# Optimization experiments

Measured on AMD Instinct MI355X. Metric: run time of the kernel, lower is better.

## Reference

```python
import jax, jax.numpy as jnp
import numpy as np

HW = 24       # image_size // patch_size
HEAD = 16     # vision num_attention_heads
B, T, C, H = 8, 8, 1024, 4096


def _sincos_1d(d, pos):
    omega = np.arange(d // 2, dtype=np.float32) / (d / 2.0)
    omega = 1.0 / 10000 ** omega
    out = np.einsum('m,d->md', pos.reshape(-1).astype(np.float32), omega)
    return np.concatenate([np.sin(out), np.cos(out)], axis=1)


def _pos_embed_3d(embed_dim, grid_size, t_size):
    ds = embed_dim // 4 * 3
    dt = embed_dim // 4
    gh = np.arange(grid_size, dtype=np.float32)
    grid = np.stack(np.meshgrid(gh, gh), axis=0).reshape(2, -1)  # (w, h) order as in source
    spatial = np.concatenate([_sincos_1d(ds // 2, grid[0]), _sincos_1d(ds // 2, grid[1])], axis=1)  # [g*g, ds]
    temporal = _sincos_1d(dt, np.arange(t_size, dtype=np.float32))  # [t, dt]
    spatial = np.repeat(spatial[np.newaxis], t_size, axis=0)                 # [t, g*g, ds]
    temporal = np.repeat(temporal[:, np.newaxis], grid_size ** 2, axis=1)    # [t, g*g, dt]
    emb = np.concatenate([temporal, spatial], axis=-1)
    return emb.reshape(1, t_size * grid_size ** 2, embed_dim).astype(np.float32)


def setup_inputs() -> dict:
    key = jax.random.key(0)
    k1, k2, k3 = jax.random.split(key, 3)
    x = jax.random.normal(k1, (B, T * HW * HW, C), dtype=jnp.float32)
    W1 = jax.random.normal(k2, (C, H), dtype=jnp.float32) * 0.02
    b1 = jnp.zeros((H,), jnp.float32)
    W2 = jax.random.normal(k3, (H, H), dtype=jnp.float32) * 0.02
    b2 = jnp.zeros((H,), jnp.float32)
    pos_embed = jnp.asarray(_pos_embed_3d(C, HW, T))
    return {"x": x, "pos_embed": pos_embed, "W1": W1, "b1": b1, "W2": W2, "b2": b2,
            "local_num_frames": T}


def _merge(x, unm_idx, src_idx, dst_idx):
    # ToMe merge: gather unmatched src tokens, scatter-add matched src into dst.
    src, dst = x[:, ::2], x[:, 1::2]
    unm = jnp.take_along_axis(src, unm_idx[:, :, None], axis=1)   # [b, t1-r, c]
    sel = jnp.take_along_axis(src, src_idx[:, :, None], axis=1)   # [b, r, c]
    dst = jax.vmap(lambda d, i, s: d.at[i].add(s))(dst, dst_idx, sel)
    return jnp.concatenate([unm, dst], axis=1)


def _merge_tokens(x, target, head):
    b, p, c = x.shape
    # static merge schedule (same logic as torch merge_tokens)
    rs, tmp = [], p
    while tmp != target:
        if tmp - target <= tmp // 2:
            rs.append(tmp - target)
            break
        rs.append(tmp // 2)
        tmp -= tmp // 2
    dim = c // head
    size = jnp.ones((b, p, 1), x.dtype)
    for r in rs:
        bb, pp, _ = x.shape
        # metric/index computation is under no_grad in the original
        metric = jax.lax.stop_gradient(x).reshape(bb, pp, head, dim).mean(2)
        metric = metric / jnp.linalg.norm(metric, axis=-1, keepdims=True)
        a_m, b_m = metric[:, ::2], metric[:, 1::2]
        scores = jnp.einsum('bic,bjc->bij', a_m, b_m)  # [b, ta, tb]
        node_max = scores.max(-1)
        node_idx = scores.argmax(-1)
        edge_idx = jnp.argsort(-node_max, axis=-1)      # descending
        unm_idx, src_idx = edge_idx[:, r:], edge_idx[:, :r]
        dst_idx = jnp.take_along_axis(node_idx, src_idx, axis=1)
        # weighted-average merge (merge_wavg)
        x = _merge(x * size, unm_idx, src_idx, dst_idx)
        size = _merge(size, unm_idx, src_idx, dst_idx)
        x = x / size
    return x


def reference(x, pos_embed, W1, b1, W2, b2, local_num_frames):
    x = x + pos_embed.astype(x.dtype)
    x = _merge_tokens(x, local_num_frames * 16, HEAD)
    h = jax.nn.gelu(x @ W1 + b1, approximate=False)  # nn.GELU() is exact erf gelu
    return h @ W2 + b2
```

## Files before the change

### kernel.cpp

```cpp
#include <hip/hip_runtime.h>
#include <hip/hip_bf16.h>
#include <math.h>
#include <stdint.h>

typedef unsigned short u16;
typedef __attribute__((ext_vector_type(8))) short short8;
typedef __attribute__((ext_vector_type(4))) float floatx4;

#define NB 8
#define P0 4608
#define C0 1024
#define H0 4096

__global__ void detect_mode_kernel(const uint32_t* __restrict__ pe_words, int* __restrict__ mode) {
  *mode = (pe_words[64] != 0u) ? 1 : 0;
}

__device__ __forceinline__ float load_in(const void* p, size_t idx, int mode) {
  if (mode) return __bfloat162float(((const __hip_bfloat16*)p)[idx]);
  return ((const float*)p)[idx];
}

__device__ __forceinline__ float4 load4(const void* p, size_t idx, int mode) {
  float4 r;
  if (mode) {
    ushort4 u = *(const ushort4*)((const u16*)p + idx);
    r.x = __bfloat162float(*(__hip_bfloat16*)&u.x);
    r.y = __bfloat162float(*(__hip_bfloat16*)&u.y);
    r.z = __bfloat162float(*(__hip_bfloat16*)&u.z);
    r.w = __bfloat162float(*(__hip_bfloat16*)&u.w);
  } else {
    r = *(const float4*)((const float*)p + idx);
  }
  return r;
}

__device__ __forceinline__ void write_hilo(u16* __restrict__ m2, size_t tok, int lane, float v) {
  __hip_bfloat16 hi = __float2bfloat16(v);
  float hif = __bfloat162float(hi);
  __hip_bfloat16 lo = __float2bfloat16(v - hif);
  m2[tok * 128 + lane] = *(u16*)&hi;
  m2[tok * 128 + 64 + lane] = *(u16*)&lo;
}

__global__ void metric_in_kernel(const void* __restrict__ x, const void* __restrict__ pos,
                                 const int* __restrict__ mode, u16* __restrict__ m2) {
  int tok = blockIdx.x * 4 + (threadIdx.x >> 6);
  int lane = threadIdx.x & 63;
  if (tok >= NB * P0) return;
  int b = tok / P0, t = tok - b * P0;
  int md = *mode;
  size_t xbase = ((size_t)b * P0 + t) * C0 + lane;
  size_t pbase = (size_t)t * C0 + lane;
  float s = 0.f;
#pragma unroll
  for (int h = 0; h < 16; ++h)
    s += load_in(x, xbase + h * 64, md) + load_in(pos, pbase + h * 64, md);
  s *= (1.f / 16.f);
  float sq = s * s;
#pragma unroll
  for (int off = 1; off < 64; off <<= 1) sq += __shfl_xor(sq, off, 64);
  write_hilo(m2, (size_t)tok, lane, s / sqrtf(sq));
}

__global__ void metric_f32_kernel(const float* __restrict__ x, u16* __restrict__ m2, int p) {
  int tok = blockIdx.x * 4 + (threadIdx.x >> 6);
  int lane = threadIdx.x & 63;
  if (tok >= NB * p) return;
  const float* xr = x + (size_t)tok * C0 + lane;
  float s = 0.f;
#pragma unroll
  for (int h = 0; h < 16; ++h) s += xr[h * 64];
  s *= (1.f / 16.f);
  float sq = s * s;
#pragma unroll
  for (int off = 1; off < 64; off <<= 1) sq += __shfl_xor(sq, off, 64);
  write_hilo(m2, (size_t)tok, lane, s / sqrtf(sq));
}

__global__ __launch_bounds__(256) void score_mfma_kernel(const u16* __restrict__ M2,
                                                         int p, int p2, int jT2,
                                                         float* __restrict__ pm,
                                                         int* __restrict__ pi) {
  const int bi = blockIdx.x, ii = blockIdx.y, b = blockIdx.z;
  const int t = threadIdx.x, w = t >> 6, L = t & 63;
  const int wr = w >> 1, wc = w & 1;
  const int fr = L & 15, fo = (L >> 4) * 8;
  const u16* Mb = M2 + (size_t)b * p * 128;

  floatx4 acc[4][4];
#pragma unroll
  for (int mt = 0; mt < 4; ++mt)
#pragma unroll
    for (int nt = 0; nt < 4; ++nt) acc[mt][nt] = (floatx4){0.f, 0.f, 0.f, 0.f};

  const u16* arp[4];
  const u16* brp[4];
#pragma unroll
  for (int mt = 0; mt < 4; ++mt) {
    int i = ii * 128 + wr * 64 + mt * 16 + fr;
    int ta = 2 * i;
    if (ta > p - 2) ta = p - 2;
    arp[mt] = Mb + (size_t)ta * 128 + fo;
    int j = bi * 128 + wc * 64 + mt * 16 + fr;
    int tb = 2 * j + 1;
    if (tb > p - 1) tb = p - 1;
    brp[mt] = Mb + (size_t)tb * 128 + fo;
  }

#pragma unroll
  for (int ks = 0; ks < 2; ++ks) {
    short8 ah[4], al[4], bh[4], bl[4];
#pragma unroll
    for (int mt = 0; mt < 4; ++mt) {
      ah[mt] = *(const short8*)(arp[mt] + ks * 32);
      al[mt] = *(const short8*)(arp[mt] + ks * 32 + 64);
      bh[mt] = *(const short8*)(brp[mt] + ks * 32);
      bl[mt] = *(const short8*)(brp[mt] + ks * 32 + 64);
    }
#pragma unroll
    for (int mt = 0; mt < 4; ++mt)
#pragma unroll
      for (int nt = 0; nt < 4; ++nt) {
        acc[mt][nt] = __builtin_amdgcn_mfma_f32_16x16x32_bf16(ah[mt], bh[nt], acc[mt][nt], 0, 0, 0);
        acc[mt][nt] = __builtin_amdgcn_mfma_f32_16x16x32_bf16(ah[mt], bl[nt], acc[mt][nt], 0, 0, 0);
        acc[mt][nt] = __builtin_amdgcn_mfma_f32_16x16x32_bf16(al[mt], bh[nt], acc[mt][nt], 0, 0, 0);
        acc[mt][nt] = __builtin_amdgcn_mfma_f32_16x16x32_bf16(al[mt], bl[nt], acc[mt][nt], 0, 0, 0);
      }
  }

  const int gi4 = (L >> 4) * 4;
#pragma unroll
  for (int mt = 0; mt < 4; ++mt) {
#pragma unroll
    for (int reg = 0; reg < 4; ++reg) {
      int i = ii * 128 + wr * 64 + mt * 16 + gi4 + reg;
      float bm = -INFINITY;
      int bj = 0x7fffffff;
#pragma unroll
      for (int nt = 0; nt < 4; ++nt) {
        int j = bi * 128 + wc * 64 + nt * 16 + fr;
        float v = acc[mt][nt][reg];
        if (j < p2 && v > bm) { bm = v; bj = j; }
      }
#pragma unroll
      for (int mk = 1; mk < 16; mk <<= 1) {
        float om = __shfl_xor(bm, mk, 64);
        int oj = __shfl_xor(bj, mk, 64);
        if (om > bm || (om == bm && oj < bj)) { bm = om; bj = oj; }
      }
      if (fr == 0 && i < p2) {
        size_t o = ((size_t)b * 2304 + i) * jT2 + bi * 2 + wc;
        pm[o] = bm;
        pi[o] = bj;
      }
    }
  }
}

__global__ void argmax_combine_kernel(const float* __restrict__ pm, const int* __restrict__ pi,
                                      int p2, int jT, float* __restrict__ nmax,
                                      int* __restrict__ nidx, int* __restrict__ head,
                                      int* __restrict__ nxt) {
  int g = blockIdx.x * 256 + threadIdx.x;
  if (g >= NB * p2) return;
  int b = g / p2, i = g - b * p2;
  const float* r = pm + ((size_t)b * 2304 + i) * jT;
  const int* ri = pi + ((size_t)b * 2304 + i) * jT;
  float best = r[0];
  int bidx = ri[0];
  for (int k = 1; k < jT; ++k) {
    if (r[k] > best || (r[k] == best && ri[k] < bidx)) { best = r[k]; bidx = ri[k]; }
  }
  nmax[g] = best;
  nidx[g] = bidx;
  int d = bidx;
  if ((unsigned)d >= (unsigned)p2) d = 0;
  nxt[g] = atomicExch(&head[(size_t)b * p2 + d], i);
}

__global__ void init_heads_kernel(int* __restrict__ h, int n) {
  int g = blockIdx.x * 256 + threadIdx.x;
  if (g < n) h[g] = -1;
}

__global__ __launch_bounds__(256) void merge_gather_in(const void* __restrict__ x,
                                                       const void* __restrict__ pos,
                                                       const int* __restrict__ mode,
                                                       const int* __restrict__ head,
                                                       const int* __restrict__ nxt,
                                                       float* __restrict__ xo,
                                                       float* __restrict__ so, int p2) {
  int tj = blockIdx.x;
  int b = tj / p2, j = tj - b * p2;
  int c = threadIdx.x * 4;
  int md = *mode;
  __shared__ int sl[64];
  __shared__ int s_n, s_cur;
  size_t xb = ((size_t)b * P0 + 2 * j + 1) * C0 + c;
  size_t pb = (size_t)(2 * j + 1) * C0 + c;
  float4 xa = load4(x, xb, md), pa = load4(pos, pb, md);
  float4 acc = {xa.x + pa.x, xa.y + pa.y, xa.z + pa.z, xa.w + pa.w};
  float cnt = 1.f;
  if (threadIdx.x == 0) s_cur = head[tj];
  __syncthreads();
  int cur = s_cur;
  while (cur != -1) {
    if (threadIdx.x == 0) {
      int n = 0, cc = cur;
      while (cc != -1 && n < 64) {
        sl[n++] = cc;
        cc = nxt[(size_t)b * p2 + cc];
      }
      s_n = n;
      s_cur = cc;
    }
    __syncthreads();
    int n = s_n;
    cur = s_cur;
    for (int k = 0; k < n; ++k) {
      int i = sl[k];
      size_t exb = ((size_t)b * P0 + 2 * i) * C0 + c;
      size_t epb = (size_t)(2 * i) * C0 + c;
      float4 ea = load4(x, exb, md), ep = load4(pos, epb, md);
      acc.x += ea.x + ep.x;
      acc.y += ea.y + ep.y;
      acc.z += ea.z + ep.z;
      acc.w += ea.w + ep.w;
      cnt += 1.f;
    }
    __syncthreads();
  }
  float inv = 1.f / cnt;
  float4 o = {acc.x * inv, acc.y * inv, acc.z * inv, acc.w * inv};
  *(float4*)(xo + (size_t)tj * C0 + c) = o;
  if (threadIdx.x == 0) so[tj] = cnt;
}

__global__ __launch_bounds__(256) void merge_gather_f(const float* __restrict__ xi,
                                                      const float* __restrict__ si,
                                                      const int* __restrict__ head,
                                                      const int* __restrict__ nxt,
                                                      float* __restrict__ xo,
                                                      float* __restrict__ so, int p, int p2) {
  int tj = blockIdx.x;
  int b = tj / p2, j = tj - b * p2;
  int c = threadIdx.x * 4;
  __shared__ int sl[64];
  __shared__ int s_n, s_cur;
  float sz = si[(size_t)b * p + 2 * j + 1];
  float4 v = *(const float4*)(xi + ((size_t)b * p + 2 * j + 1) * C0 + c);
  float4 acc = {v.x * sz, v.y * sz, v.z * sz, v.w * sz};
  float ssum = sz;
  if (threadIdx.x == 0) s_cur = head[tj];
  __syncthreads();
  int cur = s_cur;
  while (cur != -1) {
    if (threadIdx.x == 0) {
      int n = 0, cc = cur;
      while (cc != -1 && n < 64) {
        sl[n++] = cc;
        cc = nxt[(size_t)b * p2 + cc];
      }
      s_n = n;
      s_cur = cc;
    }
    __syncthreads();
    int n = s_n;
    cur = s_cur;
    for (int k = 0; k < n; ++k) {
      int i = sl[k];
      float szi = si[(size_t)b * p + 2 * i];
      float4 e = *(const float4*)(xi + ((size_t)b * p + 2 * i) * C0 + c);
      acc.x += e.x * szi;
      acc.y += e.y * szi;
      acc.z += e.z * szi;
      acc.w += e.w * szi;
      ssum += szi;
    }
    __syncthreads();
  }
  float inv = 1.f / ssum;
  float4 o = {acc.x * inv, acc.y * inv, acc.z * inv, acc.w * inv};
  *(float4*)(xo + (size_t)tj * C0 + c) = o;
  if (threadIdx.x == 0) so[tj] = ssum;
}

__global__ void rank_kernel(const float* __restrict__ nmax, const int* __restrict__ nidx,
                            int* __restrict__ unm_map, int* __restrict__ src_ord,
                            int* __restrict__ src_dst) {
  int b = blockIdx.x;
  int i = threadIdx.x;
  __shared__ float v[72];
  __shared__ int nx[72];
  if (i < 72) { v[i] = nmax[b * 72 + i]; nx[i] = nidx[b * 72 + i]; }
  __syncthreads();
  if (i < 72) {
    float vi = v[i];
    int rank = 0;
    for (int k = 0; k < 72; ++k) {
      float vk = v[k];
      rank += (vk > vi) || (vk == vi && k < i);
    }
    if (rank < 16) {
      int d = nx[i];
      if ((unsigned)d >= 72u) d = 0;
      src_ord[b * 16 + rank] = i;
      src_dst[b * 16 + rank] = d;
    } else {
      unm_map[b * 56 + (rank - 16)] = i;
    }
  }
}

__global__ void final_init(const float* __restrict__ x5, const float* __restrict__ s5,
                           const int* __restrict__ unm_map, float* __restrict__ xf,
                           float* __restrict__ sf) {
  int bt = blockIdx.x;
  int b = bt >> 7, tk = bt & 127;
  int c = threadIdx.x * 4;
  float4 o;
  float szo;
  if (tk < 56) {
    int se = unm_map[b * 56 + tk];
    if ((unsigned)se >= 72u) se = 0;
    o = *(const float4*)(x5 + ((size_t)b * 144 + 2 * se) * C0 + c);
    szo = 1.f;
  } else {
    int j = tk - 56;
    float sz = s5[b * 144 + 2 * j + 1];
    float4 v = *(const float4*)(x5 + ((size_t)b * 144 + 2 * j + 1) * C0 + c);
    o.x = v.x * sz; o.y = v.y * sz; o.z = v.z * sz; o.w = v.w * sz;
    szo = sz;
  }
  *(float4*)(xf + (size_t)bt * C0 + c) = o;
  if (threadIdx.x == 0) sf[bt] = szo;
}

__global__ void final_scatter(const float* __restrict__ x5, const float* __restrict__ s5,
                              const int* __restrict__ src_ord, const int* __restrict__ src_dst,
                              float* __restrict__ xf, float* __restrict__ sf) {
  int bk = blockIdx.x;
  int b = bk >> 4, k = bk & 15;
  int c = threadIdx.x * 4;
  int st = src_ord[b * 16 + k], dst = src_dst[b * 16 + k];
  if ((unsigned)st >= 72u) st = 0;
  if ((unsigned)dst >= 72u) dst = 0;
  float sz = s5[b * 144 + 2 * st];
  float4 v = *(const float4*)(x5 + ((size_t)b * 144 + 2 * st) * C0 + c);
  float* out = xf + ((size_t)(b * 128 + 56 + dst)) * C0 + c;
  atomicAdd(out + 0, v.x * sz);
  atomicAdd(out + 1, v.y * sz);
  atomicAdd(out + 2, v.z * sz);
  atomicAdd(out + 3, v.w * sz);
  if (threadIdx.x == 0) atomicAdd(sf + b * 128 + 56 + dst, sz);
}

__global__ void final_div_cvt(const float* __restrict__ xf, const float* __restrict__ sf,
                              __hip_bfloat16* __restrict__ xb) {
  int bt = blockIdx.x;
  int c = threadIdx.x * 4;
  float sz = sf[bt];
  float4 v = *(const float4*)(xf + (size_t)bt * C0 + c);
  __hip_bfloat16* o = xb + (size_t)bt * C0 + c;
  o[0] = __float2bfloat16(v.x / sz);
  o[1] = __float2bfloat16(v.y / sz);
  o[2] = __float2bfloat16(v.z / sz);
  o[3] = __float2bfloat16(v.w / sz);
}

__global__ void transpose_in(const void* __restrict__ in, const int* __restrict__ mode,
                             u16* __restrict__ out, int K, int N) {
  __shared__ u16 tile[64][65];
  int n0 = blockIdx.x * 64, k0 = blockIdx.y * 64;
  int t = threadIdx.x;
  int md = *mode;
  int r = t >> 4, c4 = (t & 15) * 4;
#pragma unroll
  for (int pass = 0; pass < 4; ++pass) {
    int row = r + pass * 16;
#pragma unroll
    for (int e = 0; e < 4; ++e) {
      float v = load_in(in, (size_t)(k0 + row) * N + n0 + c4 + e, md);
      __hip_bfloat16 bv = __float2bfloat16(v);
      tile[row][c4 + e] = *(u16*)&bv;
    }
  }
  __syncthreads();
#pragma unroll
  for (int pass = 0; pass < 4; ++pass) {
    int row = r + pass * 16;
    ushort4 o;
    o.x = tile[c4][row]; o.y = tile[c4 + 1][row]; o.z = tile[c4 + 2][row]; o.w = tile[c4 + 3][row];
    *(ushort4*)(out + (size_t)(n0 + row) * K + k0 + c4) = o;
  }
}

#define GL2LDS(gp, lp)                                                                   \
  __builtin_amdgcn_global_load_lds((const __attribute__((address_space(1))) uint32_t*)(gp), \
                                   (__attribute__((address_space(3))) uint32_t*)(lp), 16, 0, 0)

__global__ __launch_bounds__(256) void gemm_bt(const u16* __restrict__ A,
                                               const u16* __restrict__ BT,
                                               const void* __restrict__ bias,
                                               const int* __restrict__ mode,
                                               void* __restrict__ C, int M, int N,
                                               int K, int act, int out_sel) {
  __shared__ __align__(16) u16 As[2 * 64 * 64];
  __shared__ __align__(16) u16 Bs[2 * 128 * 64];
  const int t = threadIdx.x, w = t >> 6, L = t & 63;
  const int m0 = blockIdx.y * 64, n0 = blockIdx.x * 128;
  const int wr = w >> 1, wc = w & 1;
  const int md = *mode;
  const int fr = L & 15, fq = (L >> 4) * 8;
  const int trow = t >> 3, tc8 = (t & 7) * 8;
  floatx4 acc[2][4];
#pragma unroll
  for (int a = 0; a < 2; ++a)
#pragma unroll
    for (int bb = 0; bb < 4; ++bb) acc[a][bb] = (floatx4){0.f, 0.f, 0.f, 0.f};

  auto stage = [&](int buf, int kk) {
#pragma unroll
    for (int q = 0; q < 2; ++q)
      GL2LDS(A + (size_t)(m0 + q * 32 + trow) * K + kk + tc8,
             As + buf * 4096 + q * 2048 + t * 8);
#pragma unroll
    for (int q = 0; q < 4; ++q)
      GL2LDS(BT + (size_t)(n0 + q * 32 + trow) * K + kk + tc8,
             Bs + buf * 8192 + q * 2048 + t * 8);
  };

  stage(0, 0);
  asm volatile("s_waitcnt vmcnt(0)" ::: "memory");
  __builtin_amdgcn_s_barrier();
  int cur = 0;
  for (int k0 = 0; k0 < K; k0 += 64) {
    int kn = k0 + 64;
    if (kn < K) stage(cur ^ 1, kn);
    const u16* Ab = As + cur * 4096;
    const u16* Bb = Bs + cur * 8192;
#pragma unroll
    for (int kh = 0; kh < 2; ++kh) {
      short8 af[2], bfr[4];
#pragma unroll
      for (int mt = 0; mt < 2; ++mt)
        af[mt] = *(const short8*)(Ab + (wr * 32 + mt * 16 + fr) * 64 + kh * 32 + fq);
#pragma unroll
      for (int nt = 0; nt < 4; ++nt)
        bfr[nt] = *(const short8*)(Bb + (wc * 64 + nt * 16 + fr) * 64 + kh * 32 + fq);
#pragma unroll
      for (int mt = 0; mt < 2; ++mt)
#pragma unroll
        for (int nt = 0; nt < 4; ++nt)
          acc[mt][nt] =
              __builtin_amdgcn_mfma_f32_16x16x32_bf16(af[mt], bfr[nt], acc[mt][nt], 0, 0, 0);
    }
    asm volatile("s_waitcnt vmcnt(0)" ::: "memory");
    __builtin_amdgcn_s_barrier();
    cur ^= 1;
  }
  const int gi4 = (L >> 4) * 4;
#pragma unroll
  for (int mt = 0; mt < 2; ++mt)
#pragma unroll
    for (int nt = 0; nt < 4; ++nt) {
      int n = n0 + wc * 64 + nt * 16 + fr;
      float bz = load_in(bias, n, md);
#pragma unroll
      for (int rr = 0; rr < 4; ++rr) {
        int m = m0 + wr * 32 + mt * 16 + gi4 + rr;
        float v = acc[mt][nt][rr] + bz;
        if (act) v = 0.5f * v * (1.f + erff(v * 0.70710678118654752f));
        size_t idx = (size_t)m * N + n;
        if (out_sel == 0 || md) {
          __hip_bfloat16 bv = __float2bfloat16(v);
          ((u16*)C)[idx] = *(u16*)&bv;
        } else {
          ((float*)C)[idx] = v;
        }
      }
    }
}

extern "C" void kernel_launch(void* const* d_in, const int* in_sizes, int n_in, void* d_out,
                              int out_size, void* d_ws, size_t ws_size, hipStream_t stream) {
  const void* x = d_in[0];
  const void* pe = d_in[1];
  const void* W1 = d_in[2];
  const void* b1 = d_in[3];
  const void* W2 = d_in[4];
  const void* b2 = d_in[5];

  char* base = (char*)d_ws;
  size_t off = 0;
  auto alloc = [&](size_t bytes) -> void* {
    void* p = base + off;
    off += (bytes + 255) & ~(size_t)255;
    return p;
  };
  int* mode = (int*)alloc(256);
  u16* m2 = (u16*)alloc((size_t)NB * 4608 * 128 * 2);
  float* pm = (float*)alloc((size_t)NB * 2304 * 36 * 4);
  int* pi = (int*)alloc((size_t)NB * 2304 * 36 * 4);
  float* nmax = (float*)alloc((size_t)NB * 2304 * 4);
  int* nidx = (int*)alloc((size_t)NB * 2304 * 4);
  float* bufA = (float*)alloc((size_t)NB * 2304 * C0 * 4);
  float* bufB = (float*)alloc((size_t)NB * 1152 * C0 * 4);
  float* s1 = (float*)alloc((size_t)NB * 2304 * 4);
  float* s2 = (float*)alloc((size_t)NB * 1152 * 4);
  float* s3 = (float*)alloc((size_t)NB * 576 * 4);
  float* s4 = (float*)alloc((size_t)NB * 288 * 4);
  float* s5 = (float*)alloc((size_t)NB * 144 * 4);
  float* sf = (float*)alloc((size_t)NB * 128 * 4);
  int* unm_map = (int*)alloc((size_t)NB * 56 * 4);
  int* src_ord = (int*)alloc((size_t)NB * 16 * 4);
  int* src_dst = (int*)alloc((size_t)NB * 16 * 4);
  u16* xfb = (u16*)alloc((size_t)NB * 128 * C0 * 2);
  u16* hbuf = (u16*)alloc((size_t)1024 * H0 * 2);
  u16* w1t = (u16*)alloc((size_t)H0 * C0 * 2);
  u16* w2t = (u16*)alloc((size_t)H0 * H0 * 2);
  int* heads = (int*)alloc((size_t)NB * 4536 * 4);
  int* nxt = (int*)alloc((size_t)NB * 2304 * 4);
  if (off > ws_size) return;

  int* h_it[6];
  h_it[0] = heads;
  h_it[1] = h_it[0] + NB * 2304;
  h_it[2] = h_it[1] + NB * 1152;
  h_it[3] = h_it[2] + NB * 576;
  h_it[4] = h_it[3] + NB * 288;
  h_it[5] = h_it[4] + NB * 144;

  float* x1 = bufA;
  float* x2 = bufB;
  float* x3 = bufA;
  float* x4 = bufB;
  float* x5 = bufA;
  float* xf = bufB;

  detect_mode_kernel<<<1, 1, 0, stream>>>((const uint32_t*)pe, mode);
  init_heads_kernel<<<(NB * 4536 + 255) / 256, 256, 0, stream>>>(heads, NB * 4536);

  transpose_in<<<dim3(4096 / 64, 1024 / 64), 256, 0, stream>>>(W1, mode, w1t, 1024, 4096);
  transpose_in<<<dim3(4096 / 64, 4096 / 64), 256, 0, stream>>>(W2, mode, w2t, 4096, 4096);

  metric_in_kernel<<<NB * P0 / 4, 256, 0, stream>>>(x, pe, mode, m2);
  score_mfma_kernel<<<dim3(18, 18, NB), 256, 0, stream>>>(m2, 4608, 2304, 36, pm, pi);
  argmax_combine_kernel<<<(NB * 2304 + 255) / 256, 256, 0, stream>>>(pm, pi, 2304, 36, nmax,
                                                                     nidx, h_it[0], nxt);
  merge_gather_in<<<NB * 2304, 256, 0, stream>>>(x, pe, mode, h_it[0], nxt, x1, s1, 2304);

  float* xs_in[4] = {x1, x2, x3, x4};
  float* ss_in[4] = {s1, s2, s3, s4};
  float* xs_out[4] = {x2, x3, x4, x5};
  float* ss_out[4] = {s2, s3, s4, s5};
  int ps[5] = {2304, 1152, 576, 288, 144};
  for (int it = 0; it < 4; ++it) {
    int p = ps[it], p2 = ps[it + 1];
    int iT = (p2 + 127) / 128, jT = (p2 + 127) / 128;
    metric_f32_kernel<<<NB * p / 4, 256, 0, stream>>>(xs_in[it], m2, p);
    score_mfma_kernel<<<dim3(jT, iT, NB), 256, 0, stream>>>(m2, p, p2, 2 * jT, pm, pi);
    argmax_combine_kernel<<<(NB * p2 + 255) / 256, 256, 0, stream>>>(pm, pi, p2, 2 * jT, nmax,
                                                                     nidx, h_it[it + 1], nxt);
    merge_gather_f<<<NB * p2, 256, 0, stream>>>(xs_in[it], ss_in[it], h_it[it + 1], nxt,
                                                xs_out[it], ss_out[it], p, p2);
  }

  metric_f32_kernel<<<NB * 144 / 4, 256, 0, stream>>>(x5, m2, 144);
  score_mfma_kernel<<<dim3(1, 1, NB), 256, 0, stream>>>(m2, 144, 72, 2, pm, pi);
  argmax_combine_kernel<<<(NB * 72 + 255) / 256, 256, 0, stream>>>(pm, pi, 72, 2, nmax, nidx,
                                                                   h_it[5], nxt);
  rank_kernel<<<NB, 128, 0, stream>>>(nmax, nidx, unm_map, src_ord, src_dst);
  final_init<<<NB * 128, 256, 0, stream>>>(x5, s5, unm_map, xf, sf);
  final_scatter<<<NB * 16, 256, 0, stream>>>(x5, s5, src_ord, src_dst, xf, sf);
  final_div_cvt<<<NB * 128, 256, 0, stream>>>(xf, sf, (__hip_bfloat16*)xfb);

  gemm_bt<<<dim3(4096 / 128, 1024 / 64), 256, 0, stream>>>(xfb, w1t, b1, mode, hbuf, 1024, 4096,
                                                           1024, 1, 0);
  gemm_bt<<<dim3(4096 / 128, 1024 / 64), 256, 0, stream>>>(hbuf, w2t, b2, mode, d_out, 1024,
                                                           4096, 4096, 0, 1);
}
```

Before: 794.8 us.

## Swizzle GEMM LDS tiles and restructure async-load pipeline waits

The bf16 GEMM now stores its A and B tiles in LDS with an XOR swizzle of 16-byte column groups by row. The MFMA fragment reads, which walk 16 rows at a 128-byte stride, should then hit fewer bank conflicts. The main loop issues the next stage and waits with a partial vmcnt so only the current buffer's loads must land before the barrier. It also raises wave priority around the MFMA section and adds a min-blocks-per-CU hint of 2 to launch_bounds. The GEMMs run on only the merged tokens, so they may be a small part of total time, which limits any end-to-end effect.

```diff
diff --git a/kernel.cpp b/kernel.cpp
--- a/kernel.cpp
+++ b/kernel.cpp
@@ -400,12 +400,12 @@
   __builtin_amdgcn_global_load_lds((const __attribute__((address_space(1))) uint32_t*)(gp), \
                                    (__attribute__((address_space(3))) uint32_t*)(lp), 16, 0, 0)
 
-__global__ __launch_bounds__(256) void gemm_bt(const u16* __restrict__ A,
-                                               const u16* __restrict__ BT,
-                                               const void* __restrict__ bias,
-                                               const int* __restrict__ mode,
-                                               void* __restrict__ C, int M, int N,
-                                               int K, int act, int out_sel) {
+__global__ __launch_bounds__(256, 2) void gemm_bt(const u16* __restrict__ A,
+                                                  const u16* __restrict__ BT,
+                                                  const void* __restrict__ bias,
+                                                  const int* __restrict__ mode,
+                                                  void* __restrict__ C, int M, int N,
+                                                  int K, int act, int out_sel) {
   __shared__ __align__(16) u16 As[2 * 64 * 64];
   __shared__ __align__(16) u16 Bs[2 * 128 * 64];
   const int t = threadIdx.x, w = t >> 6, L = t & 63;
@@ -413,7 +413,6 @@
   const int wr = w >> 1, wc = w & 1;
   const int md = *mode;
   const int fr = L & 15, fq = (L >> 4) * 8;
-  const int trow = t >> 3, tc8 = (t & 7) * 8;
   floatx4 acc[2][4];
 #pragma unroll
   for (int a = 0; a < 2; ++a)
@@ -422,33 +421,48 @@
 
   auto stage = [&](int buf, int kk) {
 #pragma unroll
-    for (int q = 0; q < 2; ++q)
-      GL2LDS(A + (size_t)(m0 + q * 32 + trow) * K + kk + tc8,
-             As + buf * 4096 + q * 2048 + t * 8);
-#pragma unroll
-    for (int q = 0; q < 4; ++q)
-      GL2LDS(BT + (size_t)(n0 + q * 32 + trow) * K + kk + tc8,
-             Bs + buf * 8192 + q * 2048 + t * 8);
+    for (int q = 0; q < 2; ++q) {
+      int g = q * 256 + t;
+      int row = g >> 3, colg = (g & 7) ^ (row & 7);
+      GL2LDS(A + (size_t)(m0 + row) * K + kk + colg * 8, As + buf * 4096 + g * 8);
+    }
+#pragma unroll
+    for (int q = 0; q < 4; ++q) {
+      int g = q * 256 + t;
+      int row = g >> 3, colg = (g & 7) ^ (row & 7);
+      GL2LDS(BT + (size_t)(n0 + row) * K + kk + colg * 8, Bs + buf * 8192 + g * 8);
+    }
   };
 
   stage(0, 0);
-  asm volatile("s_waitcnt vmcnt(0)" ::: "memory");
-  __builtin_amdgcn_s_barrier();
+  const int NT = K >> 6;
   int cur = 0;
-  for (int k0 = 0; k0 < K; k0 += 64) {
-    int kn = k0 + 64;
-    if (kn < K) stage(cur ^ 1, kn);
+  for (int it = 0; it < NT; ++it) {
+    if (it + 1 < NT) {
+      stage(cur ^ 1, (it + 1) << 6);
+      asm volatile("s_waitcnt vmcnt(6)" ::: "memory");
+    } else {
+      asm volatile("s_waitcnt vmcnt(0)" ::: "memory");
+    }
+    __builtin_amdgcn_s_barrier();
     const u16* Ab = As + cur * 4096;
     const u16* Bb = Bs + cur * 8192;
+    __builtin_amdgcn_s_setprio(1);
 #pragma unroll
     for (int kh = 0; kh < 2; ++kh) {
       short8 af[2], bfr[4];
 #pragma unroll
-      for (int mt = 0; mt < 2; ++mt)
-        af[mt] = *(const short8*)(Ab + (wr * 32 + mt * 16 + fr) * 64 + kh * 32 + fq);
-#pragma unroll
-      for (int nt = 0; nt < 4; ++nt)
-        bfr[nt] = *(const short8*)(Bb + (wc * 64 + nt * 16 + fr) * 64 + kh * 32 + fq);
+      for (int mt = 0; mt < 2; ++mt) {
+        int ra = wr * 32 + mt * 16 + fr;
+        int cg = (kh * 4 + (L >> 4)) ^ (ra & 7);
+        af[mt] = *(const short8*)(Ab + ra * 64 + cg * 8);
+      }
+#pragma unroll
+      for (int nt = 0; nt < 4; ++nt) {
+        int rb = wc * 64 + nt * 16 + fr;
+        int cg = (kh * 4 + (L >> 4)) ^ (rb & 7);
+        bfr[nt] = *(const short8*)(Bb + rb * 64 + cg * 8);
+      }
 #pragma unroll
       for (int mt = 0; mt < 2; ++mt)
 #pragma unroll
@@ -456,7 +470,7 @@
           acc[mt][nt] =
               __builtin_amdgcn_mfma_f32_16x16x32_bf16(af[mt], bfr[nt], acc[mt][nt], 0, 0, 0);
     }
-    asm volatile("s_waitcnt vmcnt(0)" ::: "memory");
+    __builtin_amdgcn_s_setprio(0);
     __builtin_amdgcn_s_barrier();
     cur ^= 1;
   }
```

After: 782.1 us. Within noise of the previous version (-1.6%).
